# Kernel optimization log

Hardware: AMD Instinct MI355X
Metric: run time of the kernel (lower is better)

The kernel has to match this reference:

```python
import jax, jax.numpy as jnp
import numpy as np
from jax import lax

B, T, V, L = 256, 512, 256, 64
EPS = 1e-7  # keras backend epsilon used by ctc_batch_cost
NEG = -1e30  # log(0) surrogate, safe in float32


def setup_inputs() -> dict:
    key = jax.random.key(0)
    k1, k2 = jax.random.split(key)
    # labels in [0, V-1): class V-1 is reserved for the CTC blank
    y_true = jax.random.randint(k1, (B, L), 0, V - 1)
    # ctc_batch_cost expects probabilities (softmax output)
    logits = jax.random.normal(k2, (B, T, V), dtype=jnp.float32)
    y_pred = jax.nn.softmax(logits, axis=-1)
    return {"y_true": y_true, "y_pred": y_pred}


def reference(y_true, y_pred):
    """Keras ctc_batch_cost: per-example CTC negative log-likelihood, shape [B,1].

    Matches TF semantics: blank = V-1, log(y_pred + eps), full input/label lengths,
    merge-repeated forward DP in log space.
    """
    b, t, v = y_pred.shape
    l = y_true.shape[1]
    S = 2 * l + 1  # extended label: blank-interleaved
    blank = v - 1

    logp = jnp.log(y_pred + EPS)  # [B,T,V]

    # extended label sequence z: blank at even positions, labels at odd
    ext = jnp.full((b, S), blank, dtype=y_true.dtype).at[:, 1::2].set(y_true)  # [B,S]

    # lp[b,t,s] = logp[b,t,ext[b,s]]
    idx = jnp.broadcast_to(ext[:, None, :], (b, t, S))
    lp = jnp.take_along_axis(logp, idx, axis=2)  # [B,T,S]

    # skip transition s-2 -> s allowed iff z[s] != blank and z[s] != z[s-2]
    ext_m2 = jnp.concatenate([jnp.full((b, 2), -1, dtype=ext.dtype), ext[:, :-2]], axis=1)
    skip = (ext != blank) & (ext != ext_m2)  # [B,S]

    # alpha at t=0: only first blank or first label reachable
    alpha0 = jnp.full((b, S), NEG, dtype=logp.dtype)
    alpha0 = alpha0.at[:, 0].set(lp[:, 0, 0]).at[:, 1].set(lp[:, 0, 1])

    neg1 = jnp.full((b, 1), NEG, dtype=logp.dtype)
    neg2 = jnp.full((b, 2), NEG, dtype=logp.dtype)

    def step(alpha, lpt):
        a1 = jnp.concatenate([neg1, alpha[:, :-1]], axis=1)
        a2 = jnp.concatenate([neg2, alpha[:, :-2]], axis=1)
        m = jnp.logaddexp(alpha, a1)
        m = jnp.where(skip, jnp.logaddexp(m, a2), m)
        return m + lpt, None

    lp_t = jnp.moveaxis(lp[:, 1:], 1, 0)  # [T-1, B, S] time-major
    alphaT, _ = lax.scan(step, alpha0, lp_t)

    loss = -jnp.logaddexp(alphaT[:, -1], alphaT[:, -2])  # [B]
    return loss[:, None]
```

## Files before the change

### kernel.cpp

```cpp
#include <hip/hip_runtime.h>
#include <math.h>


#define BB   256
#define TI   512
#define VV   256
#define LL   64
#define CH   32
#define NCH  (TI / CH)
#define EPSF 1e-7f
#define LN2F 0.6931471805599453f

#if __has_builtin(__builtin_amdgcn_logf)
__device__ __forceinline__ float flog2(float x) { return __builtin_amdgcn_logf(x); }
#else
__device__ __forceinline__ float flog2(float x) { return __log2f(x); }
#endif

template <int CTRL>
__device__ __forceinline__ float dppf(float oldv, float v) {
    return __int_as_float(__builtin_amdgcn_update_dpp(
        __float_as_int(oldv), __float_as_int(v), CTRL, 0xF, 0xF, false));
}
__device__ __forceinline__ float shup0(float x) { return dppf<0x138>(0.0f, x); }

struct DP {
    float a0, a1, a128;
    float C;
    float f, fs;
    float skipf;
    int   lane;
};

__device__ __forceinline__ void rescale(DP& d) {
    float m  = fmaxf(fmaxf(d.a0, d.a1), d.a128);
    int   mi    = __float_as_int(m);
    int   ebits = mi & 0x7f800000;
    bool  dead  = (ebits == 0);
    float s = __int_as_float((254 << 23) - ebits);
    s = dead ? 1.0f : s;
    d.a0 *= s; d.a1 *= s; d.a128 *= s;
    float Ei  = (float)((mi >> 23) - 127);
    float Cm1 = shup0(d.C);
    d.C = dead ? Cm1 : (d.C + Ei);
    float Cm1b = shup0(d.C);
    int dCi = (int)(Cm1b - d.C);
    int e = dCi + 127;
    e = e < 0 ? 0 : (e > 254 ? 254 : e);
    float fn = __int_as_float(e << 23);
    d.f  = (d.lane == 0) ? 0.0f : fn;
    d.fs = d.f * d.skipf;
}

__device__ __forceinline__ void dp_step(DP& d, float pb, float pl) {
    float pa1 = shup0(d.a1);
    float s01 = d.a0 + d.a1;
    float na0   = fmaf(pa1, d.f,  d.a0) * pb;
    float na1   = fmaf(pa1, d.fs, s01)  * pl;
    float na128 = (d.a128 + d.a1) * pb;
    d.a0 = na0; d.a1 = na1; d.a128 = na128;
}

template <bool PA, bool FIRST>
__device__ __forceinline__ void dp_chunk(DP& d, const float (&pb)[CH],
                                         const float (&pl)[CH]) {
    #pragma unroll
    for (int tt = 0; tt < CH; ++tt) {
        if (FIRST && tt == 0) {
            d.a0 = (d.lane == 0) ? pb[0] : 0.0f;
            d.a1 = (d.lane == 0) ? pl[0] : 0.0f;
        } else {
            dp_step(d, pb[tt], pl[tt]);
        }
        if (PA || (tt & 7) == 7) rescale(d);
    }
}

__device__ __forceinline__ void fill_chunk(const float* __restrict__ src,
                                           int lab, int cc, int lane,
                                           float* __restrict__ pbuf,
                                           float* __restrict__ lbuf) {
    const float* rowbase = src + (size_t)cc * CH * VV;
    const int r = lane & 31;
    float bv = rowbase[r * VV + (VV - 1)];
    float lv[CH];
    #pragma unroll
    for (int i = 0; i < CH; ++i)
        lv[i] = rowbase[i * VV + lab];
    if (lane < 32) pbuf[r] = bv + EPSF;
    #pragma unroll
    for (int i = 0; i < CH; ++i)
        lbuf[i * 64 + lane] = lv[i] + EPSF;
}

__global__ __launch_bounds__(128) void ctc_kernel(
        const int* __restrict__ y_true,
        const float* __restrict__ y_pred,
        float* __restrict__ out) {
    __shared__ float pbuf[4][CH];
    __shared__ float lbuf[4][CH * 64];

    const int b    = blockIdx.x;
    const int tid  = threadIdx.x;
    const int lane = tid & 63;
    const int wave = tid >> 6;
    const float* src = y_pred + (size_t)b * TI * VV;

    const int lab = y_true[b * LL + lane];

    DP d;
    d.lane = lane;
    {
        const int prevLab = __shfl_up(lab, 1);
        d.skipf = (lane == 0 || lab != prevLab) ? 1.0f : 0.0f;
    }
    d.a0 = 0.0f; d.a1 = 0.0f; d.a128 = 0.0f;
    d.C = 0.0f; d.f = 0.0f; d.fs = 0.0f;

    if (wave == 1) {
        fill_chunk(src, lab, 0, lane, pbuf[0], lbuf[0]);
        fill_chunk(src, lab, 1, lane, pbuf[1], lbuf[1]);
    }
    __syncthreads();

    for (int c = 0; c < NCH; ++c) {
        if (wave == 1) {
            if (c + 2 < NCH)
                fill_chunk(src, lab, c + 2, lane,
                           pbuf[(c + 2) & 3], lbuf[(c + 2) & 3]);
        } else {
            float pb[CH], pl[CH];
            const float* pp = pbuf[c & 3];
            const float* ll = lbuf[c & 3] + lane;
            #pragma unroll
            for (int i = 0; i < CH; ++i) {
                pb[i] = pp[i];
                pl[i] = ll[i * 64];
            }
            if (c == 0)      dp_chunk<true,  true >(d, pb, pl);
            else if (c < 4)  dp_chunk<true,  false>(d, pb, pl);
            else             dp_chunk<false, false>(d, pb, pl);
        }
        __syncthreads();
    }

    if (wave == 0 && lane == 63) {
        float tail = fmaxf(d.a128 + d.a1, 1e-37f);
        out[b] = -LN2F * (d.C + flog2(tail));
    }
}

extern "C" void kernel_launch(void* const* d_in, const int* in_sizes, int n_in,
                              void* d_out, int out_size, void* d_ws, size_t ws_size,
                              hipStream_t stream) {
    const int*   y_true = (const int*)d_in[0];
    const float* y_pred = (const float*)d_in[1];
    float*       out    = (float*)d_out;
    ctc_kernel<<<dim3(BB), dim3(128), 0, stream>>>(y_true, y_pred, out);
}
```

Before: 196.2 us.

## Stage full probability rows into LDS via direct global-to-LDS loads

The producer wave no longer gathers the label and blank columns through registers. It issues coalesced 16-byte global_load_lds transfers that copy entire 32-row chunks into a 4-slot LDS ring. The consumer wave then picks the blank and label entries from LDS and adds epsilon itself. This is meant to cut the producer's per-element gather latency and register round-trips, at the cost of a 128KB LDS footprint that limits residency to one block per CU. It also relies on the asynchronous LDS writes finishing before the barriers that hand each slot to the consumer.

```diff
diff --git a/kernel.cpp b/kernel.cpp
--- a/kernel.cpp
+++ b/kernel.cpp
@@ -8,6 +8,7 @@
 #define LL   64
 #define CH   32
 #define NCH  (TI / CH)
+#define RING 4
 #define EPSF 1e-7f
 #define LN2F 0.6931471805599453f
 
@@ -76,29 +77,24 @@
     }
 }
 
-__device__ __forceinline__ void fill_chunk(const float* __restrict__ src,
-                                           int lab, int cc, int lane,
-                                           float* __restrict__ pbuf,
-                                           float* __restrict__ lbuf) {
-    const float* rowbase = src + (size_t)cc * CH * VV;
-    const int r = lane & 31;
-    float bv = rowbase[r * VV + (VV - 1)];
-    float lv[CH];
+__device__ __forceinline__ void stage_chunk(const float* __restrict__ src,
+                                            int cc, int lane,
+                                            float* __restrict__ lslot) {
+    const float* g = src + (size_t)cc * CH * VV + lane * 4;
     #pragma unroll
-    for (int i = 0; i < CH; ++i)
-        lv[i] = rowbase[i * VV + lab];
-    if (lane < 32) pbuf[r] = bv + EPSF;
-    #pragma unroll
-    for (int i = 0; i < CH; ++i)
-        lbuf[i * 64 + lane] = lv[i] + EPSF;
+    for (int r = 0; r < CH; ++r) {
+        __builtin_amdgcn_global_load_lds(
+            (const __attribute__((address_space(1))) void*)(g + r * VV),
+            (__attribute__((address_space(3))) void*)(lslot + r * VV),
+            16, 0, 0);
+    }
 }
 
 __global__ __launch_bounds__(128) void ctc_kernel(
         const int* __restrict__ y_true,
         const float* __restrict__ y_pred,
         float* __restrict__ out) {
-    __shared__ float pbuf[4][CH];
-    __shared__ float lbuf[4][CH * 64];
+    __shared__ float ring[RING][CH * VV];
 
     const int b    = blockIdx.x;
     const int tid  = threadIdx.x;
@@ -118,24 +114,22 @@
     d.C = 0.0f; d.f = 0.0f; d.fs = 0.0f;
 
     if (wave == 1) {
-        fill_chunk(src, lab, 0, lane, pbuf[0], lbuf[0]);
-        fill_chunk(src, lab, 1, lane, pbuf[1], lbuf[1]);
+        stage_chunk(src, 0, lane, ring[0]);
+        stage_chunk(src, 1, lane, ring[1]);
     }
     __syncthreads();
 
     for (int c = 0; c < NCH; ++c) {
         if (wave == 1) {
             if (c + 2 < NCH)
-                fill_chunk(src, lab, c + 2, lane,
-                           pbuf[(c + 2) & 3], lbuf[(c + 2) & 3]);
+                stage_chunk(src, c + 2, lane, ring[(c + 2) & (RING - 1)]);
         } else {
+            const float* base = ring[c & (RING - 1)];
             float pb[CH], pl[CH];
-            const float* pp = pbuf[c & 3];
-            const float* ll = lbuf[c & 3] + lane;
             #pragma unroll
             for (int i = 0; i < CH; ++i) {
-                pb[i] = pp[i];
-                pl[i] = ll[i * 64];
+                pb[i] = base[i * VV + (VV - 1)] + EPSF;
+                pl[i] = base[i * VV + lab]      + EPSF;
             }
             if (c == 0)      dp_chunk<true,  true >(d, pb, pl);
             else if (c < 4)  dp_chunk<true,  false>(d, pb, pl);
```

New measurement: 196.0 us. Within noise of the previous version (-0.1%).
